# Performance work log

Measured on AMD Instinct MI355X. Metric: run time of the kernel, lower is better.

Reference implementation:

```python
import jax, jax.numpy as jnp
import numpy as np

N = 50000      # nodes
E = 800000     # edges (avg degree 16)
IN = 256       # in_features
HD = 4         # num_heads
D = 64         # out_features per head


def setup_inputs() -> dict:
    key = jax.random.key(0)
    k1, k2, k3, k4, k5 = jax.random.split(key, 5)
    h = jax.random.normal(k1, (N, IN), dtype=jnp.float32)
    edge_index = jax.random.randint(k2, (2, E), 0, N)
    # W stored as [in_features, num_heads*out_features] (h @ W == Linear(h))
    W = jax.random.normal(k3, (IN, HD * D), dtype=jnp.float32) * (1.0 / np.sqrt(IN))
    a_src = jax.random.normal(k4, (HD, D), dtype=jnp.float32) * 0.1
    a_dst = jax.random.normal(k5, (HD, D), dtype=jnp.float32) * 0.1
    return {"h": h, "edge_index": edge_index, "W": W, "a_src": a_src, "a_dst": a_dst}


def reference(h, edge_index, W, a_src, a_dst):
    n = h.shape[0]
    src, dst = edge_index[0], edge_index[1]
    # project: [N, H, D]
    hp = (h @ W).reshape(n, HD, D)
    # per-edge attention logits [E, H]
    e_src = jnp.einsum('ehd,hd->eh', hp[src], a_src)
    e_dst = jnp.einsum('ehd,hd->eh', hp[dst], a_dst)
    e = jax.nn.leaky_relu(e_src + e_dst, negative_slope=0.2)
    # segment softmax over incoming edges of each dst node
    e_max = jax.ops.segment_max(e, dst, num_segments=n)          # [N, H]
    ex = jnp.exp(e - e_max[dst])                                  # [E, H]
    e_sum = jax.ops.segment_sum(ex, dst, num_segments=n)         # [N, H]
    alpha = ex / (e_sum[dst] + 1e-16)                             # [E, H]
    # weighted aggregation
    msg = hp[src] * alpha[..., None]                              # [E, H, D]
    out = jax.ops.segment_sum(msg, dst, num_segments=n)          # [N, H, D]
    return out.reshape(n, HD * D)                                 # concat=True
```

## Files before the change

kernel.cpp:

```cpp
#include <hip/hip_runtime.h>

#define HD 4
#define D 64
#define NHD 256
#define N_IN 256

typedef __attribute__((ext_vector_type(8))) __bf16 bf16x8;
typedef __attribute__((ext_vector_type(4))) __bf16 bf16x4;
typedef __attribute__((ext_vector_type(4))) float f32x4;

__global__ void wsplit_kernel(const float* __restrict__ W, __bf16* __restrict__ WtH,
                              __bf16* __restrict__ WtL) {
  const int k = blockIdx.x, n = threadIdx.x;
  float w = W[k * NHD + n];
  __bf16 hi = (__bf16)w;
  __bf16 lo = (__bf16)(w - (float)hi);
  WtH[n * N_IN + k] = hi;
  WtL[n * N_IN + k] = lo;
}

constexpr int AROW = 40;

__global__ __launch_bounds__(256) void gemm_mfma_kernel(
    const float* __restrict__ A, const __bf16* __restrict__ WtH,
    const __bf16* __restrict__ WtL, const float* __restrict__ a_src,
    const float* __restrict__ a_dst, __bf16* __restrict__ hp16,
    float* __restrict__ s_out, float* __restrict__ t_out, int M) {
  __shared__ __bf16 As[128 * AROW];
  __shared__ __bf16 BsH[128 * AROW];
  __shared__ __bf16 BsL[128 * AROW];
  const int tid = threadIdx.x;
  const int lane = tid & 63, wv = tid >> 6;
  const int wr = wv >> 1, wc = wv & 1;
  const int c15 = lane & 15, quad = lane >> 4;
  const int m0 = blockIdx.x * 128, n0 = blockIdx.y * 128;

  f32x4 acc[4][4];
#pragma unroll
  for (int i = 0; i < 4; ++i)
#pragma unroll
    for (int j = 0; j < 4; ++j) acc[i][j] = (f32x4){0.f, 0.f, 0.f, 0.f};

  const int am = tid >> 1, aks = (tid & 1) * 16;
  const int gr = m0 + am;
  const bool arow_ok = (gr < M);
  const float* Arow = &A[(size_t)gr * N_IN];
  const __bf16* BHrow = &WtH[(size_t)(n0 + am) * N_IN];
  const __bf16* BLrow = &WtL[(size_t)(n0 + am) * N_IN];

  for (int kc = 0; kc < 8; ++kc) {
    const int k0 = kc * 32;
    float4 f0, f1, f2, f3;
    if (arow_ok) {
      f0 = *(const float4*)&Arow[k0 + aks + 0];
      f1 = *(const float4*)&Arow[k0 + aks + 4];
      f2 = *(const float4*)&Arow[k0 + aks + 8];
      f3 = *(const float4*)&Arow[k0 + aks + 12];
    } else {
      f0 = f1 = f2 = f3 = make_float4(0.f, 0.f, 0.f, 0.f);
    }
    bf16x8 bh0 = *(const bf16x8*)&BHrow[k0 + aks];
    bf16x8 bh1 = *(const bf16x8*)&BHrow[k0 + aks + 8];
    bf16x8 bl0 = *(const bf16x8*)&BLrow[k0 + aks];
    bf16x8 bl1 = *(const bf16x8*)&BLrow[k0 + aks + 8];

    __syncthreads();
    bf16x8 a0, a1;
    a0[0] = (__bf16)f0.x; a0[1] = (__bf16)f0.y; a0[2] = (__bf16)f0.z; a0[3] = (__bf16)f0.w;
    a0[4] = (__bf16)f1.x; a0[5] = (__bf16)f1.y; a0[6] = (__bf16)f1.z; a0[7] = (__bf16)f1.w;
    a1[0] = (__bf16)f2.x; a1[1] = (__bf16)f2.y; a1[2] = (__bf16)f2.z; a1[3] = (__bf16)f2.w;
    a1[4] = (__bf16)f3.x; a1[5] = (__bf16)f3.y; a1[6] = (__bf16)f3.z; a1[7] = (__bf16)f3.w;
    *(bf16x8*)&As[am * AROW + aks + 0] = a0;
    *(bf16x8*)&As[am * AROW + aks + 8] = a1;
    *(bf16x8*)&BsH[am * AROW + aks + 0] = bh0;
    *(bf16x8*)&BsH[am * AROW + aks + 8] = bh1;
    *(bf16x8*)&BsL[am * AROW + aks + 0] = bl0;
    *(bf16x8*)&BsL[am * AROW + aks + 8] = bl1;
    __syncthreads();

    bf16x8 af[4], bfh[4], bfl[4];
#pragma unroll
    for (int i = 0; i < 4; ++i) {
      af[i]  = *(bf16x8*)&As[(wr * 64 + i * 16 + c15) * AROW + quad * 8];
      bfh[i] = *(bf16x8*)&BsH[(wc * 64 + i * 16 + c15) * AROW + quad * 8];
      bfl[i] = *(bf16x8*)&BsL[(wc * 64 + i * 16 + c15) * AROW + quad * 8];
    }
#pragma unroll
    for (int mi = 0; mi < 4; ++mi)
#pragma unroll
      for (int ni = 0; ni < 4; ++ni)
        acc[mi][ni] = __builtin_amdgcn_mfma_f32_16x16x32_bf16(af[mi], bfh[ni], acc[mi][ni], 0, 0, 0);
#pragma unroll
    for (int mi = 0; mi < 4; ++mi)
#pragma unroll
      for (int ni = 0; ni < 4; ++ni)
        acc[mi][ni] = __builtin_amdgcn_mfma_f32_16x16x32_bf16(af[mi], bfl[ni], acc[mi][ni], 0, 0, 0);
  }

  const int head = blockIdx.y * 2 + wc;
  float av[4], ad[4];
#pragma unroll
  for (int ni = 0; ni < 4; ++ni) {
    av[ni] = a_src[head * D + ni * 16 + c15];
    ad[ni] = a_dst[head * D + ni * 16 + c15];
  }
  const int row0w = m0 + wr * 64;
#pragma unroll
  for (int mi = 0; mi < 4; ++mi) {
#pragma unroll
    for (int j = 0; j < 4; ++j) {
      float ps = acc[mi][0][j] * av[0] + acc[mi][1][j] * av[1] +
                 acc[mi][2][j] * av[2] + acc[mi][3][j] * av[3];
      float pt = acc[mi][0][j] * ad[0] + acc[mi][1][j] * ad[1] +
                 acc[mi][2][j] * ad[2] + acc[mi][3][j] * ad[3];
#pragma unroll
      for (int m = 1; m < 16; m <<= 1) {
        ps += __shfl_xor(ps, m);
        pt += __shfl_xor(pt, m);
      }
      const int row = row0w + mi * 16 + quad * 4 + j;
      if (c15 == 0 && row < M) {
        s_out[row * HD + head] = ps;
        t_out[row * HD + head] = pt;
      }
    }
#pragma unroll
    for (int ni = 0; ni < 4; ++ni) {
#pragma unroll
      for (int j = 0; j < 4; ++j) {
        const int row = row0w + mi * 16 + quad * 4 + j;
        const int col = n0 + wc * 64 + ni * 16 + c15;
        if (row < M) hp16[(size_t)row * NHD + col] = (__bf16)acc[mi][ni][j];
      }
    }
  }
}

__global__ void init_kernel(int* __restrict__ deg, int n) {
  int i = blockIdx.x * blockDim.x + threadIdx.x;
  if (i < n) deg[i] = 0;
}

__global__ void degree_kernel(const int* __restrict__ ei, int* __restrict__ deg, int E) {
  int e = blockIdx.x * blockDim.x + threadIdx.x;
  if (e < E) atomicAdd(&deg[ei[E + e]], 1);
}

__global__ __launch_bounds__(256) void scan1_kernel(const int* __restrict__ deg,
                                                    int* __restrict__ partial,
                                                    int* __restrict__ blocksum, int n) {
  __shared__ int ws[4];
  const int tid = threadIdx.x, lane = tid & 63, wv = tid >> 6;
  const int base = blockIdx.x * 1024 + tid * 4;
  int v0 = (base + 0 < n) ? deg[base + 0] : 0;
  int v1 = (base + 1 < n) ? deg[base + 1] : 0;
  int v2 = (base + 2 < n) ? deg[base + 2] : 0;
  int v3 = (base + 3 < n) ? deg[base + 3] : 0;
  int sum = v0 + v1 + v2 + v3;
  int incl = sum;
#pragma unroll
  for (int off = 1; off < 64; off <<= 1) {
    int y = __shfl_up(incl, off);
    if (lane >= off) incl += y;
  }
  if (lane == 63) ws[wv] = incl;
  __syncthreads();
  int wbase = 0;
#pragma unroll
  for (int w = 0; w < 4; ++w)
    if (w < wv) wbase += ws[w];
  int excl = wbase + incl - sum;
  if (base + 0 < n) partial[base + 0] = excl;
  if (base + 1 < n) partial[base + 1] = excl + v0;
  if (base + 2 < n) partial[base + 2] = excl + v0 + v1;
  if (base + 3 < n) partial[base + 3] = excl + v0 + v1 + v2;
  if (tid == 0) {
    __syncthreads();
  }
  if (tid == 255) blocksum[blockIdx.x] = wbase + incl;
}

__global__ __launch_bounds__(64) void scan2_kernel(const int* __restrict__ blocksum,
                                                   int* __restrict__ blockoff,
                                                   int* __restrict__ row_ptr_n, int nb) {
  const int lane = threadIdx.x;
  int v = (lane < nb) ? blocksum[lane] : 0;
  int incl = v;
#pragma unroll
  for (int off = 1; off < 64; off <<= 1) {
    int y = __shfl_up(incl, off);
    if (lane >= off) incl += y;
  }
  if (lane < nb) blockoff[lane] = incl - v;
  if (lane == 63) *row_ptr_n = incl;
}

__global__ __launch_bounds__(256) void scan3_kernel(const int* __restrict__ partial,
                                                    const int* __restrict__ blockoff,
                                                    int* __restrict__ row_ptr,
                                                    int* __restrict__ cursor, int n) {
  const int base = blockIdx.x * 1024 + threadIdx.x * 4;
  const int off = blockoff[blockIdx.x];
  if (base + 3 < n) {
    int4 p = *(const int4*)&partial[base];
    int4 r = make_int4(p.x + off, p.y + off, p.z + off, p.w + off);
    *(int4*)&row_ptr[base] = r;
    *(int4*)&cursor[base] = r;
  } else {
    for (int j = 0; j < 4; ++j)
      if (base + j < n) {
        int r = partial[base + j] + off;
        row_ptr[base + j] = r;
        cursor[base + j] = r;
      }
  }
}

__global__ void scatter_kernel(const int* __restrict__ ei, int* __restrict__ cursor,
                               int* __restrict__ csr_src, int E) {
  int e = blockIdx.x * blockDim.x + threadIdx.x;
  if (e >= E) return;
  int sn = ei[e], dn = ei[E + e];
  int pos = atomicAdd(&cursor[dn], 1);
  csr_src[pos] = sn;
}

__global__ __launch_bounds__(256) void aggregate_kernel(
    const int* __restrict__ row_ptr, const int* __restrict__ csr_src,
    const float* __restrict__ s, const float* __restrict__ t,
    const __bf16* __restrict__ hp16, float* __restrict__ out, int N) {
  const int wave = threadIdx.x >> 6;
  const int lane = threadIdx.x & 63;
  const int node = blockIdx.x * 4 + wave;
  if (node >= N) return;
  const int h = lane >> 4;
  const int d0 = lane * 4;
  const int beg = row_ptr[node], end = row_ptr[node + 1];
  const float tn = t[node * HD + h];
  float num0 = 0.f, num1 = 0.f, num2 = 0.f, num3 = 0.f, den = 0.f;
  int i = beg;
  for (; i + 4 <= end; i += 4) {
    int sn0 = csr_src[i], sn1 = csr_src[i + 1], sn2 = csr_src[i + 2], sn3 = csr_src[i + 3];
    bf16x4 v0 = *(const bf16x4*)&hp16[(size_t)sn0 * NHD + d0];
    bf16x4 v1 = *(const bf16x4*)&hp16[(size_t)sn1 * NHD + d0];
    bf16x4 v2 = *(const bf16x4*)&hp16[(size_t)sn2 * NHD + d0];
    bf16x4 v3 = *(const bf16x4*)&hp16[(size_t)sn3 * NHD + d0];
    float lg0 = s[sn0 * HD + h] + tn;
    float lg1 = s[sn1 * HD + h] + tn;
    float lg2 = s[sn2 * HD + h] + tn;
    float lg3 = s[sn3 * HD + h] + tn;
    lg0 = fmaxf(lg0, 0.2f * lg0);
    lg1 = fmaxf(lg1, 0.2f * lg1);
    lg2 = fmaxf(lg2, 0.2f * lg2);
    lg3 = fmaxf(lg3, 0.2f * lg3);
    float ex0 = __expf(lg0), ex1 = __expf(lg1), ex2 = __expf(lg2), ex3 = __expf(lg3);
    den += (ex0 + ex1) + (ex2 + ex3);
    num0 += ex0 * (float)v0[0] + ex1 * (float)v1[0] + ex2 * (float)v2[0] + ex3 * (float)v3[0];
    num1 += ex0 * (float)v0[1] + ex1 * (float)v1[1] + ex2 * (float)v2[1] + ex3 * (float)v3[1];
    num2 += ex0 * (float)v0[2] + ex1 * (float)v1[2] + ex2 * (float)v2[2] + ex3 * (float)v3[2];
    num3 += ex0 * (float)v0[3] + ex1 * (float)v1[3] + ex2 * (float)v2[3] + ex3 * (float)v3[3];
  }
  for (; i < end; ++i) {
    int sn0 = csr_src[i];
    bf16x4 v0 = *(const bf16x4*)&hp16[(size_t)sn0 * NHD + d0];
    float lg0 = s[sn0 * HD + h] + tn;
    lg0 = fmaxf(lg0, 0.2f * lg0);
    float ex0 = __expf(lg0);
    den += ex0;
    num0 += ex0 * (float)v0[0];
    num1 += ex0 * (float)v0[1];
    num2 += ex0 * (float)v0[2];
    num3 += ex0 * (float)v0[3];
  }
  const float inv = 1.0f / (den + 1e-16f);
  float4 o = make_float4(num0 * inv, num1 * inv, num2 * inv, num3 * inv);
  *(float4*)&out[(size_t)node * NHD + d0] = o;
}

extern "C" void kernel_launch(void* const* d_in, const int* in_sizes, int n_in,
                              void* d_out, int out_size, void* d_ws, size_t ws_size,
                              hipStream_t stream) {
  const float* h_ptr  = (const float*)d_in[0];
  const int*   ei     = (const int*)d_in[1];
  const float* W      = (const float*)d_in[2];
  const float* a_src  = (const float*)d_in[3];
  const float* a_dst  = (const float*)d_in[4];
  float* out = (float*)d_out;

  const int N = in_sizes[0] / N_IN;
  const int E = in_sizes[1] / 2;
  const int NB = (N + 1023) / 1024;

  auto align256 = [](size_t x) { return (x + 255) & ~size_t(255); };
  char* base = (char*)d_ws;
  size_t off = 0;
  __bf16* hp16 = (__bf16*)(base + off);  off += align256((size_t)N * NHD * 2);
  __bf16* WtH  = (__bf16*)(base + off);  off += align256((size_t)N_IN * NHD * 2);
  __bf16* WtL  = (__bf16*)(base + off);  off += align256((size_t)N_IN * NHD * 2);
  float* s       = (float*)(base + off); off += align256((size_t)N * HD * 4);
  float* t       = (float*)(base + off); off += align256((size_t)N * HD * 4);
  int*   deg     = (int*)(base + off);   off += align256((size_t)N * 4);
  int*   partial = (int*)(base + off);   off += align256((size_t)N * 4);
  int*   blocksum= (int*)(base + off);   off += align256((size_t)NB * 4);
  int*   blockoff= (int*)(base + off);   off += align256((size_t)NB * 4);
  int*   row_ptr = (int*)(base + off);   off += align256((size_t)(N + 1) * 4);
  int*   cursor  = (int*)(base + off);   off += align256((size_t)N * 4);
  int*   csr_src = (int*)(base + off);   off += align256((size_t)E * 4);

  init_kernel<<<(N + 255) / 256, 256, 0, stream>>>(deg, N);
  wsplit_kernel<<<N_IN, NHD, 0, stream>>>(W, WtH, WtL);
  {
    dim3 grid((N + 127) / 128, NHD / 128);
    gemm_mfma_kernel<<<grid, 256, 0, stream>>>(h_ptr, WtH, WtL, a_src, a_dst, hp16, s, t, N);
  }
  degree_kernel<<<(E + 255) / 256, 256, 0, stream>>>(ei, deg, E);
  scan1_kernel<<<NB, 256, 0, stream>>>(deg, partial, blocksum, N);
  scan2_kernel<<<1, 64, 0, stream>>>(blocksum, blockoff, &row_ptr[N], NB);
  scan3_kernel<<<NB, 256, 0, stream>>>(partial, blockoff, row_ptr, cursor, N);
  scatter_kernel<<<(E + 255) / 256, 256, 0, stream>>>(ei, cursor, csr_src, E);
  aggregate_kernel<<<(N + 3) / 4, 256, 0, stream>>>(row_ptr, csr_src, s, t, hp16, out, N);
}
```

Baseline: 292.0 us.

## Merge preprocessing kernels into fewer launches and unroll aggregation by eight

Folds the weight split and degree counting into one launch. The first-level degree scan becomes extra blocks of the GEMM launch, and the second and third scan levels merge into one kernel, cutting the launch count from nine to five plus a memset. Each block of the merged scan kernel recomputes the small block-sum scan redundantly. The aggregation loop is unrolled from four to eight edges to raise memory-level parallelism, at the cost of more registers. The scan blocks occupy the first block indices of the GEMM grid, so they may not overlap much with GEMM work.

```diff
diff --git a/kernel.cpp b/kernel.cpp
--- a/kernel.cpp
+++ b/kernel.cpp
@@ -9,31 +9,76 @@
 typedef __attribute__((ext_vector_type(4))) __bf16 bf16x4;
 typedef __attribute__((ext_vector_type(4))) float f32x4;
 
-__global__ void wsplit_kernel(const float* __restrict__ W, __bf16* __restrict__ WtH,
-                              __bf16* __restrict__ WtL) {
-  const int k = blockIdx.x, n = threadIdx.x;
-  float w = W[k * NHD + n];
-  __bf16 hi = (__bf16)w;
-  __bf16 lo = (__bf16)(w - (float)hi);
-  WtH[n * N_IN + k] = hi;
-  WtL[n * N_IN + k] = lo;
-}
-
 constexpr int AROW = 40;
 
-__global__ __launch_bounds__(256) void gemm_mfma_kernel(
+__global__ __launch_bounds__(256) void pre_kernel(const float* __restrict__ W,
+                                                  __bf16* __restrict__ WtH,
+                                                  __bf16* __restrict__ WtL,
+                                                  const int* __restrict__ ei,
+                                                  int* __restrict__ deg, int E) {
+  const int b = blockIdx.x;
+  if (b < N_IN) {
+    const int k = b, n = threadIdx.x;
+    float w = W[k * NHD + n];
+    __bf16 hi = (__bf16)w;
+    __bf16 lo = (__bf16)(w - (float)hi);
+    WtH[n * N_IN + k] = hi;
+    WtL[n * N_IN + k] = lo;
+  } else {
+    const int e = (b - N_IN) * 256 + threadIdx.x;
+    if (e < E) atomicAdd(&deg[ei[E + e]], 1);
+  }
+}
+
+__global__ __launch_bounds__(256) void gemm_scan_kernel(
     const float* __restrict__ A, const __bf16* __restrict__ WtH,
     const __bf16* __restrict__ WtL, const float* __restrict__ a_src,
     const float* __restrict__ a_dst, __bf16* __restrict__ hp16,
-    float* __restrict__ s_out, float* __restrict__ t_out, int M) {
+    float* __restrict__ s_out, float* __restrict__ t_out, int M,
+    const int* __restrict__ deg, int* __restrict__ partial,
+    int* __restrict__ blocksum, int NB, int MT) {
   __shared__ __bf16 As[128 * AROW];
   __shared__ __bf16 BsH[128 * AROW];
   __shared__ __bf16 BsL[128 * AROW];
+  __shared__ int ws4[4];
   const int tid = threadIdx.x;
+
+  if ((int)blockIdx.x < NB) {
+    const int lane = tid & 63, wv = tid >> 6;
+    const int base = blockIdx.x * 1024 + tid * 4;
+    const int n = M;
+    int v0 = (base + 0 < n) ? deg[base + 0] : 0;
+    int v1 = (base + 1 < n) ? deg[base + 1] : 0;
+    int v2 = (base + 2 < n) ? deg[base + 2] : 0;
+    int v3 = (base + 3 < n) ? deg[base + 3] : 0;
+    int sum = v0 + v1 + v2 + v3;
+    int incl = sum;
+#pragma unroll
+    for (int off = 1; off < 64; off <<= 1) {
+      int y = __shfl_up(incl, off);
+      if (lane >= off) incl += y;
+    }
+    if (lane == 63) ws4[wv] = incl;
+    __syncthreads();
+    int wbase = 0;
+#pragma unroll
+    for (int w = 0; w < 4; ++w)
+      if (w < wv) wbase += ws4[w];
+    int excl = wbase + incl - sum;
+    if (base + 0 < n) partial[base + 0] = excl;
+    if (base + 1 < n) partial[base + 1] = excl + v0;
+    if (base + 2 < n) partial[base + 2] = excl + v0 + v1;
+    if (base + 3 < n) partial[base + 3] = excl + v0 + v1 + v2;
+    if (tid == 255) blocksum[blockIdx.x] = wbase + incl;
+    return;
+  }
+
+  const int g = blockIdx.x - NB;
+  const int bx = g % MT, by = g / MT;
   const int lane = tid & 63, wv = tid >> 6;
   const int wr = wv >> 1, wc = wv & 1;
   const int c15 = lane & 15, quad = lane >> 4;
-  const int m0 = blockIdx.x * 128, n0 = blockIdx.y * 128;
+  const int m0 = bx * 128, n0 = by * 128;
 
   f32x4 acc[4][4];
 #pragma unroll
@@ -97,7 +142,7 @@
         acc[mi][ni] = __builtin_amdgcn_mfma_f32_16x16x32_bf16(af[mi], bfl[ni], acc[mi][ni], 0, 0, 0);
   }
 
-  const int head = blockIdx.y * 2 + wc;
+  const int head = by * 2 + wc;
   float av[4], ad[4];
 #pragma unroll
   for (int ni = 0; ni < 4; ++ni) {
@@ -136,71 +181,28 @@
   }
 }
 
-__global__ void init_kernel(int* __restrict__ deg, int n) {
-  int i = blockIdx.x * blockDim.x + threadIdx.x;
-  if (i < n) deg[i] = 0;
-}
-
-__global__ void degree_kernel(const int* __restrict__ ei, int* __restrict__ deg, int E) {
-  int e = blockIdx.x * blockDim.x + threadIdx.x;
-  if (e < E) atomicAdd(&deg[ei[E + e]], 1);
-}
-
-__global__ __launch_bounds__(256) void scan1_kernel(const int* __restrict__ deg,
-                                                    int* __restrict__ partial,
-                                                    int* __restrict__ blocksum, int n) {
-  __shared__ int ws[4];
-  const int tid = threadIdx.x, lane = tid & 63, wv = tid >> 6;
+__global__ __launch_bounds__(256) void scan23_kernel(const int* __restrict__ partial,
+                                                     const int* __restrict__ blocksum,
+                                                     int* __restrict__ row_ptr,
+                                                     int* __restrict__ cursor, int n, int NB) {
+  __shared__ int s_off;
+  const int tid = threadIdx.x;
+  if (tid < 64) {
+    int v = (tid < NB) ? blocksum[tid] : 0;
+    int incl = v;
+#pragma unroll
+    for (int off = 1; off < 64; off <<= 1) {
+      int y = __shfl_up(incl, off);
+      if (tid >= off) incl += y;
+    }
+    int prev = __shfl_up(incl, 1);
+    int excl = (tid == 0) ? 0 : prev;
+    if (tid == (int)blockIdx.x) s_off = excl;
+    if (blockIdx.x == 0 && tid == NB - 1) row_ptr[n] = incl;
+  }
+  __syncthreads();
+  const int off = s_off;
   const int base = blockIdx.x * 1024 + tid * 4;
-  int v0 = (base + 0 < n) ? deg[base + 0] : 0;
-  int v1 = (base + 1 < n) ? deg[base + 1] : 0;
-  int v2 = (base + 2 < n) ? deg[base + 2] : 0;
-  int v3 = (base + 3 < n) ? deg[base + 3] : 0;
-  int sum = v0 + v1 + v2 + v3;
-  int incl = sum;
-#pragma unroll
-  for (int off = 1; off < 64; off <<= 1) {
-    int y = __shfl_up(incl, off);
-    if (lane >= off) incl += y;
-  }
-  if (lane == 63) ws[wv] = incl;
-  __syncthreads();
-  int wbase = 0;
-#pragma unroll
-  for (int w = 0; w < 4; ++w)
-    if (w < wv) wbase += ws[w];
-  int excl = wbase + incl - sum;
-  if (base + 0 < n) partial[base + 0] = excl;
-  if (base + 1 < n) partial[base + 1] = excl + v0;
-  if (base + 2 < n) partial[base + 2] = excl + v0 + v1;
-  if (base + 3 < n) partial[base + 3] = excl + v0 + v1 + v2;
-  if (tid == 0) {
-    __syncthreads();
-  }
-  if (tid == 255) blocksum[blockIdx.x] = wbase + incl;
-}
-
-__global__ __launch_bounds__(64) void scan2_kernel(const int* __restrict__ blocksum,
-                                                   int* __restrict__ blockoff,
-                                                   int* __restrict__ row_ptr_n, int nb) {
-  const int lane = threadIdx.x;
-  int v = (lane < nb) ? blocksum[lane] : 0;
-  int incl = v;
-#pragma unroll
-  for (int off = 1; off < 64; off <<= 1) {
-    int y = __shfl_up(incl, off);
-    if (lane >= off) incl += y;
-  }
-  if (lane < nb) blockoff[lane] = incl - v;
-  if (lane == 63) *row_ptr_n = incl;
-}
-
-__global__ __launch_bounds__(256) void scan3_kernel(const int* __restrict__ partial,
-                                                    const int* __restrict__ blockoff,
-                                                    int* __restrict__ row_ptr,
-                                                    int* __restrict__ cursor, int n) {
-  const int base = blockIdx.x * 1024 + threadIdx.x * 4;
-  const int off = blockoff[blockIdx.x];
   if (base + 3 < n) {
     int4 p = *(const int4*)&partial[base];
     int4 r = make_int4(p.x + off, p.y + off, p.z + off, p.w + off);
@@ -239,26 +241,36 @@
   const float tn = t[node * HD + h];
   float num0 = 0.f, num1 = 0.f, num2 = 0.f, num3 = 0.f, den = 0.f;
   int i = beg;
-  for (; i + 4 <= end; i += 4) {
+  for (; i + 8 <= end; i += 8) {
     int sn0 = csr_src[i], sn1 = csr_src[i + 1], sn2 = csr_src[i + 2], sn3 = csr_src[i + 3];
+    int sn4 = csr_src[i + 4], sn5 = csr_src[i + 5], sn6 = csr_src[i + 6], sn7 = csr_src[i + 7];
     bf16x4 v0 = *(const bf16x4*)&hp16[(size_t)sn0 * NHD + d0];
     bf16x4 v1 = *(const bf16x4*)&hp16[(size_t)sn1 * NHD + d0];
     bf16x4 v2 = *(const bf16x4*)&hp16[(size_t)sn2 * NHD + d0];
     bf16x4 v3 = *(const bf16x4*)&hp16[(size_t)sn3 * NHD + d0];
-    float lg0 = s[sn0 * HD + h] + tn;
-    float lg1 = s[sn1 * HD + h] + tn;
-    float lg2 = s[sn2 * HD + h] + tn;
-    float lg3 = s[sn3 * HD + h] + tn;
-    lg0 = fmaxf(lg0, 0.2f * lg0);
-    lg1 = fmaxf(lg1, 0.2f * lg1);
-    lg2 = fmaxf(lg2, 0.2f * lg2);
-    lg3 = fmaxf(lg3, 0.2f * lg3);
+    bf16x4 v4 = *(const bf16x4*)&hp16[(size_t)sn4 * NHD + d0];
+    bf16x4 v5 = *(const bf16x4*)&hp16[(size_t)sn5 * NHD + d0];
+    bf16x4 v6 = *(const bf16x4*)&hp16[(size_t)sn6 * NHD + d0];
+    bf16x4 v7 = *(const bf16x4*)&hp16[(size_t)sn7 * NHD + d0];
+    float lg0 = s[sn0 * HD + h] + tn, lg1 = s[sn1 * HD + h] + tn;
+    float lg2 = s[sn2 * HD + h] + tn, lg3 = s[sn3 * HD + h] + tn;
+    float lg4 = s[sn4 * HD + h] + tn, lg5 = s[sn5 * HD + h] + tn;
+    float lg6 = s[sn6 * HD + h] + tn, lg7 = s[sn7 * HD + h] + tn;
+    lg0 = fmaxf(lg0, 0.2f * lg0); lg1 = fmaxf(lg1, 0.2f * lg1);
+    lg2 = fmaxf(lg2, 0.2f * lg2); lg3 = fmaxf(lg3, 0.2f * lg3);
+    lg4 = fmaxf(lg4, 0.2f * lg4); lg5 = fmaxf(lg5, 0.2f * lg5);
+    lg6 = fmaxf(lg6, 0.2f * lg6); lg7 = fmaxf(lg7, 0.2f * lg7);
     float ex0 = __expf(lg0), ex1 = __expf(lg1), ex2 = __expf(lg2), ex3 = __expf(lg3);
-    den += (ex0 + ex1) + (ex2 + ex3);
-    num0 += ex0 * (float)v0[0] + ex1 * (float)v1[0] + ex2 * (float)v2[0] + ex3 * (float)v3[0];
-    num1 += ex0 * (float)v0[1] + ex1 * (float)v1[1] + ex2 * (float)v2[1] + ex3 * (float)v3[1];
-    num2 += ex0 * (float)v0[2] + ex1 * (float)v1[2] + ex2 * (float)v2[2] + ex3 * (float)v3[2];
-    num3 += ex0 * (float)v0[3] + ex1 * (float)v1[3] + ex2 * (float)v2[3] + ex3 * (float)v3[3];
+    float ex4 = __expf(lg4), ex5 = __expf(lg5), ex6 = __expf(lg6), ex7 = __expf(lg7);
+    den += ((ex0 + ex1) + (ex2 + ex3)) + ((ex4 + ex5) + (ex6 + ex7));
+    num0 += ex0 * (float)v0[0] + ex1 * (float)v1[0] + ex2 * (float)v2[0] + ex3 * (float)v3[0]
+          + ex4 * (float)v4[0] + ex5 * (float)v5[0] + ex6 * (float)v6[0] + ex7 * (float)v7[0];
+    num1 += ex0 * (float)v0[1] + ex1 * (float)v1[1] + ex2 * (float)v2[1] + ex3 * (float)v3[1]
+          + ex4 * (float)v4[1] + ex5 * (float)v5[1] + ex6 * (float)v6[1] + ex7 * (float)v7[1];
+    num2 += ex0 * (float)v0[2] + ex1 * (float)v1[2] + ex2 * (float)v2[2] + ex3 * (float)v3[2]
+          + ex4 * (float)v4[2] + ex5 * (float)v5[2] + ex6 * (float)v6[2] + ex7 * (float)v7[2];
+    num3 += ex0 * (float)v0[3] + ex1 * (float)v1[3] + ex2 * (float)v2[3] + ex3 * (float)v3[3]
+          + ex4 * (float)v4[3] + ex5 * (float)v5[3] + ex6 * (float)v6[3] + ex7 * (float)v7[3];
   }
   for (; i < end; ++i) {
     int sn0 = csr_src[i];
@@ -290,6 +302,7 @@
   const int N = in_sizes[0] / N_IN;
   const int E = in_sizes[1] / 2;
   const int NB = (N + 1023) / 1024;
+  const int MT = (N + 127) / 128;
 
   auto align256 = [](size_t x) { return (x + 255) & ~size_t(255); };
   char* base = (char*)d_ws;
@@ -302,21 +315,16 @@
   int*   deg     = (int*)(base + off);   off += align256((size_t)N * 4);
   int*   partial = (int*)(base + off);   off += align256((size_t)N * 4);
   int*   blocksum= (int*)(base + off);   off += align256((size_t)NB * 4);
-  int*   blockoff= (int*)(base + off);   off += align256((size_t)NB * 4);
   int*   row_ptr = (int*)(base + off);   off += align256((size_t)(N + 1) * 4);
   int*   cursor  = (int*)(base + off);   off += align256((size_t)N * 4);
   int*   csr_src = (int*)(base + off);   off += align256((size_t)E * 4);
 
-  init_kernel<<<(N + 255) / 256, 256, 0, stream>>>(deg, N);
-  wsplit_kernel<<<N_IN, NHD, 0, stream>>>(W, WtH, WtL);
-  {
-    dim3 grid((N + 127) / 128, NHD / 128);
-    gemm_mfma_kernel<<<grid, 256, 0, stream>>>(h_ptr, WtH, WtL, a_src, a_dst, hp16, s, t, N);
-  }
-  degree_kernel<<<(E + 255) / 256, 256, 0, stream>>>(ei, deg, E);
-  scan1_kernel<<<NB, 256, 0, stream>>>(deg, partial, blocksum, N);
-  scan2_kernel<<<1, 64, 0, stream>>>(blocksum, blockoff, &row_ptr[N], NB);
-  scan3_kernel<<<NB, 256, 0, stream>>>(partial, blockoff, row_ptr, cursor, N);
+  hipMemsetAsync(deg, 0, (size_t)N * 4, stream);
+  pre_kernel<<<N_IN + (E + 255) / 256, 256, 0, stream>>>(W, WtH, WtL, ei, deg, E);
+  gemm_scan_kernel<<<NB + MT * 2, 256, 0, stream>>>(h_ptr, WtH, WtL, a_src, a_dst,
+                                                    hp16, s, t, N, deg, partial,
+                                                    blocksum, NB, MT);
+  scan23_kernel<<<NB, 256, 0, stream>>>(partial, blocksum, row_ptr, cursor, N, NB);
   scatter_kernel<<<(E + 255) / 256, 256, 0, stream>>>(ei, cursor, csr_src, E);
   aggregate_kernel<<<(N + 3) / 4, 256, 0, stream>>>(row_ptr, csr_src, s, t, hp16, out, N);
 }
```

Measured after the change: 291.4 us. No clear change (-0.2%).
